# Kernel tuning notes

Measured on AMD Instinct MI355X. Metric: run time of the kernel, lower is better.

Reference implementation:

```python
import jax, jax.numpy as jnp
import numpy as np

N_NODES = 50000
HID = 256


def _gcn_norm(edge_index, n_nodes):
    # PyG GCNConv default: add self-loops, symmetric normalization
    src, dst = edge_index[0], edge_index[1]
    loop = jnp.arange(n_nodes, dtype=src.dtype)
    src = jnp.concatenate([src, loop])
    dst = jnp.concatenate([dst, loop])
    deg = jax.ops.segment_sum(jnp.ones_like(src, dtype=jnp.float32), dst, num_segments=n_nodes)
    dinv = jnp.where(deg > 0, jax.lax.rsqrt(jnp.maximum(deg, 1.0)), 0.0)
    norm = dinv[src] * dinv[dst]  # [E + N]
    return src, dst, norm


def _gcn_conv(x, W, b, src, dst, norm, n_nodes):
    h = x @ W                                   # [N, H] dense transform first (PyG order)
    msg = h[src] * norm[:, None]                # gather + scale
    out = jax.ops.segment_sum(msg, dst, num_segments=n_nodes)
    return out + b


def setup_inputs() -> dict:
    key = jax.random.key(0)
    ks = jax.random.split(key, 8)
    x = jax.random.normal(ks[0], (N_NODES, HID), dtype=jnp.float32)
    edge_index = jax.random.randint(ks[1], (2, 1600000), 0, N_NODES, dtype=jnp.int64)
    s = 1.0 / np.sqrt(HID)
    W1 = jax.random.normal(ks[2], (HID, HID), dtype=jnp.float32) * s
    b1 = jnp.zeros((HID,), dtype=jnp.float32)
    Wmu = jax.random.normal(ks[3], (HID, HID), dtype=jnp.float32) * s
    bmu = jnp.zeros((HID,), dtype=jnp.float32)
    Wls = jax.random.normal(ks[4], (HID, HID), dtype=jnp.float32) * s * 0.1
    bls = jnp.zeros((HID,), dtype=jnp.float32)
    return {"x": x, "edge_index": edge_index, "W1": W1, "b1": b1,
            "Wmu": Wmu, "bmu": bmu, "Wls": Wls, "bls": bls}


def reference(x, edge_index, W1, b1, Wmu, bmu, Wls, bls):
    n = x.shape[0]
    src, dst, norm = _gcn_norm(edge_index, n)
    h = jax.nn.relu(_gcn_conv(x, W1, b1, src, dst, norm, n))
    mu = _gcn_conv(h, Wmu, bmu, src, dst, norm, n)
    logstd = _gcn_conv(h, Wls, bls, src, dst, norm, n)
    std = jnp.exp(logstd)
    eps = jax.random.normal(jax.random.key(1), std.shape, dtype=std.dtype)
    z = mu + std * eps
    return (z, mu, logstd)
```

## Files before the change

kernel.cpp:

```cpp
#include <hip/hip_runtime.h>
#include <stdint.h>

#define HID 256

typedef __bf16 bf16x8 __attribute__((ext_vector_type(8)));
typedef float  f32x4  __attribute__((ext_vector_type(4)));
typedef unsigned int uint4v __attribute__((ext_vector_type(4)));

__device__ __forceinline__ unsigned short f2bf(float f){
  unsigned int x = __float_as_uint(f);
  x += 0x7FFFu + ((x >> 16) & 1u);
  return (unsigned short)(x >> 16);
}
__device__ __forceinline__ float bf2f(unsigned int u){
  return __uint_as_float(u << 16);
}
__device__ __forceinline__ bf16x8 ntload8(const unsigned short* p){
  uint4v t = __builtin_nontemporal_load((const uint4v*)p);
  return __builtin_bit_cast(bf16x8, t);
}

__global__ void count_kernel(const int* __restrict__ ei, int E, int* __restrict__ deg){
  int e = blockIdx.x*256 + threadIdx.x;
  if (e < E) atomicAdd(&deg[ei[E + e]], 1);
}

__global__ void dinv_kernel(const int* __restrict__ deg, float* __restrict__ dinv, int N){
  int i = blockIdx.x*256 + threadIdx.x;
  if (i < N) dinv[i] = 1.0f / sqrtf((float)(deg[i] + 1));
}

__global__ void scan1_kernel(const int* __restrict__ deg, int* __restrict__ rowptr,
                             int* __restrict__ partials, int N){
  __shared__ int sm[256];
  int t = threadIdx.x;
  int i = blockIdx.x*256 + t;
  int v = (i < N) ? deg[i] : 0;
  int acc = v;
  sm[t] = acc;
  __syncthreads();
  for (int off = 1; off < 256; off <<= 1){
    int add = (t >= off) ? sm[t - off] : 0;
    __syncthreads();
    acc += add;
    sm[t] = acc;
    __syncthreads();
  }
  if (i < N) rowptr[i] = acc - v;
  if (t == 255) partials[blockIdx.x] = acc;
}

__global__ void scan2_kernel(int* __restrict__ partials, int nb){
  __shared__ int sm[256];
  int t = threadIdx.x;
  int v = (t < nb) ? partials[t] : 0;
  int acc = v;
  sm[t] = acc;
  __syncthreads();
  for (int off = 1; off < 256; off <<= 1){
    int add = (t >= off) ? sm[t - off] : 0;
    __syncthreads();
    acc += add;
    sm[t] = acc;
    __syncthreads();
  }
  if (t < nb) partials[t] = acc - v;
}

__global__ void scan3_kernel(int* __restrict__ rowptr, const int* __restrict__ partials,
                             int N, int E){
  int i = blockIdx.x*256 + threadIdx.x;
  if (i < N) rowptr[i] += partials[blockIdx.x];
  if (i == 0) rowptr[N] = E;
}

__global__ void scatter_kernel(const int* __restrict__ ei, int E, const int* __restrict__ rowptr,
                               int* __restrict__ fill, const float* __restrict__ dinv,
                               int* __restrict__ col, float* __restrict__ wgt){
  int e = blockIdx.x*256 + threadIdx.x;
  if (e >= E) return;
  int s = ei[e];
  int d = ei[E + e];
  int p = rowptr[d] + atomicAdd(&fill[d], 1);
  col[p] = s;
  wgt[p] = dinv[s] * dinv[d];
}

__global__ void convX_kernel(const float* __restrict__ x, unsigned short* __restrict__ xb, int total8){
  int t = blockIdx.x*256 + threadIdx.x;
  if (t >= total8) return;
  const float* p = x + (size_t)t*8;
  f32x4 a = *(const f32x4*)p;
  f32x4 b = *(const f32x4*)(p + 4);
  ushort4 o0, o1;
  o0.x = f2bf(a[0]); o0.y = f2bf(a[1]); o0.z = f2bf(a[2]); o0.w = f2bf(a[3]);
  o1.x = f2bf(b[0]); o1.y = f2bf(b[1]); o1.z = f2bf(b[2]); o1.w = f2bf(b[3]);
  ushort4* q = (ushort4*)(xb + (size_t)t*8);
  q[0] = o0; q[1] = o1;
}

__global__ void convW_kernel(const float* __restrict__ W1, const float* __restrict__ Wmu,
                             const float* __restrict__ Wls, unsigned short* __restrict__ Wt){
  int t = blockIdx.x*256 + threadIdx.x;
  if (t >= 3*65536) return;
  int m = t >> 16;
  int r = t & 0xFFFF;
  int n = r >> 8, k = r & 255;
  int ksrc = (m == 0) ? k : ((k & ~63) | ((k & 3) << 4) | ((k >> 2) & 15));
  const float* W = (m == 0) ? W1 : (m == 1 ? Wmu : Wls);
  Wt[t] = f2bf(W[ksrc*HID + n]);
}

__global__ void agg_bf16(const unsigned short* __restrict__ X, unsigned short* __restrict__ Y,
                         const int* __restrict__ rowptr, const int* __restrict__ col,
                         const float* __restrict__ wgt, const float* __restrict__ dinv,
                         int N, int sin, int sout){
  int w = (blockIdx.x * blockDim.x + threadIdx.x) >> 6;
  int lane = threadIdx.x & 63;
  if (w >= N) return;
  float sd = dinv[w];
  f32x4 acc;
  {
    uint2 u = *((const uint2*)(X + (size_t)w*sin) + lane);
    float s2 = sd*sd;
    acc[0] = bf2f(u.x & 0xFFFFu) * s2;
    acc[1] = bf2f(u.x >> 16)     * s2;
    acc[2] = bf2f(u.y & 0xFFFFu) * s2;
    acc[3] = bf2f(u.y >> 16)     * s2;
  }
  int p0 = rowptr[w], p1 = rowptr[w+1];
  for (int base = p0; base < p1; base += 64){
    int idx = base + lane;
    int   sc = 0;  float wc = 0.f;
    if (idx < p1){ sc = col[idx]; wc = wgt[idx]; }
    int cnt = min(p1 - base, 64);
    for (int j = 0; j < cnt; ++j){
      int   s = __shfl(sc, j);
      float f = __shfl(wc, j);
      uint2 u = *((const uint2*)(X + (size_t)s*sin) + lane);
      acc[0] = fmaf(bf2f(u.x & 0xFFFFu), f, acc[0]);
      acc[1] = fmaf(bf2f(u.x >> 16),     f, acc[1]);
      acc[2] = fmaf(bf2f(u.y & 0xFFFFu), f, acc[2]);
      acc[3] = fmaf(bf2f(u.y >> 16),     f, acc[3]);
    }
  }
  ushort4 o;
  o.x = f2bf(acc[0]); o.y = f2bf(acc[1]); o.z = f2bf(acc[2]); o.w = f2bf(acc[3]);
  *((ushort4*)(Y + (size_t)w*sout) + lane) = o;
}

__global__ __launch_bounds__(256, 4) void gemm1_kernel(const unsigned short* __restrict__ A,
    const unsigned short* __restrict__ Bt, const float* __restrict__ bias,
    unsigned short* __restrict__ H, int N){
  int r0 = blockIdx.x * 32;
  int lane = threadIdx.x & 63;
  int nw = threadIdx.x >> 6;
  int lr = lane & 15, kg = lane >> 4;
  f32x4 acc[2][4] = {};
  for (int ks = 0; ks < 8; ++ks){
    int kb = ks*32 + kg*8;
    bf16x8 af[2];
    #pragma unroll
    for (int rf = 0; rf < 2; ++rf){
      int row = r0 + rf*16 + lr; if (row > N-1) row = N-1;
      af[rf] = *(const bf16x8*)(A + (size_t)row*HID + kb);
    }
    #pragma unroll
    for (int cf = 0; cf < 4; ++cf){
      int c = nw*64 + cf*16 + lr;
      bf16x8 bfr = *(const bf16x8*)(Bt + (size_t)c*HID + kb);
      acc[0][cf] = __builtin_amdgcn_mfma_f32_16x16x32_bf16(af[0], bfr, acc[0][cf], 0, 0, 0);
      acc[1][cf] = __builtin_amdgcn_mfma_f32_16x16x32_bf16(af[1], bfr, acc[1][cf], 0, 0, 0);
    }
  }
  float bv[4];
  #pragma unroll
  for (int cf = 0; cf < 4; ++cf) bv[cf] = bias[nw*64 + cf*16 + lr];
  #pragma unroll
  for (int rf = 0; rf < 2; ++rf){
    #pragma unroll
    for (int i = 0; i < 4; ++i){
      int row = r0 + rf*16 + kg*4 + i;
      if (row < N){
        ushort4 o;
        o.x = f2bf(fmaxf(acc[rf][0][i] + bv[0], 0.0f));
        o.y = f2bf(fmaxf(acc[rf][1][i] + bv[1], 0.0f));
        o.z = f2bf(fmaxf(acc[rf][2][i] + bv[2], 0.0f));
        o.w = f2bf(fmaxf(acc[rf][3][i] + bv[3], 0.0f));
        *(ushort4*)(H + (size_t)row*HID + nw*64 + lr*4) = o;
      }
    }
  }
}

__device__ __forceinline__ unsigned int rotl32(unsigned int v, int r){
  return (v << r) | (v >> (32 - r));
}

__device__ __forceinline__ float gauss_eps(unsigned int idxv){
  unsigned int x0 = 0u, x1 = idxv;
  const unsigned int ks0 = 0u, ks1 = 1u, ks2 = 0x1BD11BDAu ^ 0u ^ 1u;
  x0 += ks0; x1 += ks1;
#define TFR(r) { x0 += x1; x1 = rotl32(x1, r); x1 ^= x0; }
  TFR(13) TFR(15) TFR(26) TFR(6)   x0 += ks1; x1 += ks2 + 1u;
  TFR(17) TFR(29) TFR(16) TFR(24)  x0 += ks2; x1 += ks0 + 2u;
  TFR(13) TFR(15) TFR(26) TFR(6)   x0 += ks0; x1 += ks1 + 3u;
  TFR(17) TFR(29) TFR(16) TFR(24)  x0 += ks1; x1 += ks2 + 4u;
  TFR(13) TFR(15) TFR(26) TFR(6)   x0 += ks2; x1 += ks0 + 5u;
#undef TFR
  unsigned int bits = x0 ^ x1;
  float f = __uint_as_float((bits >> 9) | 0x3F800000u) - 1.0f;
  const float lo = -0.99999994f;
  float u = fmaxf(lo, fmaf(f, 2.0f, lo));
  float t = fmaf(-u, u, 1.0f);
  float wv = -0.69314718056f * __builtin_amdgcn_logf(t);
  float p;
  if (wv < 5.0f){
    wv -= 2.5f;
    p = 2.81022636e-08f;
    p = fmaf(p, wv, 3.43273939e-07f);
    p = fmaf(p, wv, -3.5233877e-06f);
    p = fmaf(p, wv, -4.39150654e-06f);
    p = fmaf(p, wv, 0.00021858087f);
    p = fmaf(p, wv, -0.00125372503f);
    p = fmaf(p, wv, -0.00417768164f);
    p = fmaf(p, wv, 0.246640727f);
    p = fmaf(p, wv, 1.50140941f);
  } else {
    wv = sqrtf(wv) - 3.0f;
    p = -0.000200214257f;
    p = fmaf(p, wv, 0.000100950558f);
    p = fmaf(p, wv, 0.00134934322f);
    p = fmaf(p, wv, -0.00367342844f);
    p = fmaf(p, wv, 0.00573950773f);
    p = fmaf(p, wv, -0.0076224613f);
    p = fmaf(p, wv, 0.00943887047f);
    p = fmaf(p, wv, 1.00167406f);
    p = fmaf(p, wv, 2.83297682f);
  }
  return 1.4142135381698608f * (p * u);
}

__global__ __launch_bounds__(256, 4) void gemm23_kernel(const unsigned short* __restrict__ A2b,
    const unsigned short* __restrict__ Btm, const unsigned short* __restrict__ Btl,
    const float* __restrict__ bmu, const float* __restrict__ bls,
    float* __restrict__ Z, float* __restrict__ MU, float* __restrict__ LS, int N){
  __shared__ float sml[2][16][260];
  int r0 = blockIdx.x * 32;
  int lane = threadIdx.x & 63;
  int nw = threadIdx.x >> 6;
  int lr = lane & 15, kg = lane >> 4;
  f32x4 am[2][4] = {};
  f32x4 al[2][4] = {};
  for (int ks = 0; ks < 8; ++ks){
    int kb = ks*32 + kg*8;
    bf16x8 af[2];
    #pragma unroll
    for (int rf = 0; rf < 2; ++rf){
      int row = r0 + rf*16 + lr; if (row > N-1) row = N-1;
      af[rf] = ntload8(A2b + (size_t)row*512 + kb);
    }
    #pragma unroll
    for (int cf = 0; cf < 4; ++cf){
      int c = nw*64 + cf*16 + lr;
      bf16x8 bm_ = *(const bf16x8*)(Btm + (size_t)c*HID + kb);
      bf16x8 bl_ = *(const bf16x8*)(Btl + (size_t)c*HID + kb);
      am[0][cf] = __builtin_amdgcn_mfma_f32_16x16x32_bf16(af[0], bm_, am[0][cf], 0, 0, 0);
      am[1][cf] = __builtin_amdgcn_mfma_f32_16x16x32_bf16(af[1], bm_, am[1][cf], 0, 0, 0);
      al[0][cf] = __builtin_amdgcn_mfma_f32_16x16x32_bf16(af[0], bl_, al[0][cf], 0, 0, 0);
      al[1][cf] = __builtin_amdgcn_mfma_f32_16x16x32_bf16(af[1], bl_, al[1][cf], 0, 0, 0);
    }
  }
  f32x4 bm4 = *(const f32x4*)(bmu + lane*4);
  f32x4 bl4 = *(const f32x4*)(bls + lane*4);
  for (int rf = 0; rf < 2; ++rf){
    #pragma unroll
    for (int cf = 0; cf < 4; ++cf){
      int c = nw*64 + cf*16 + lr;
      #pragma unroll
      for (int i = 0; i < 4; ++i){
        int rl = kg*4 + i;
        sml[0][rl][c] = am[rf][cf][i];
        sml[1][rl][c] = al[rf][cf][i];
      }
    }
    __syncthreads();
    #pragma unroll
    for (int rr = 0; rr < 4; ++rr){
      int rl = nw*4 + rr;
      int row = r0 + rf*16 + rl;
      if (row < N){
        f32x4 m4 = *(const f32x4*)&sml[0][rl][lane*4];
        f32x4 l4 = *(const f32x4*)&sml[1][rl][lane*4];
        m4 += bm4;
        l4 += bl4;
        size_t base = (size_t)row*HID + lane*4;
        f32x4 z4;
        #pragma unroll
        for (int j = 0; j < 4; ++j){
          float e = gauss_eps((unsigned int)(base + j));
          float s = __builtin_amdgcn_exp2f(l4[j] * 1.44269504f);
          z4[j] = fmaf(s, e, m4[j]);
        }
        __builtin_nontemporal_store(z4, (f32x4*)(Z  + base));
        __builtin_nontemporal_store(m4, (f32x4*)(MU + base));
        __builtin_nontemporal_store(l4, (f32x4*)(LS + base));
      }
    }
    __syncthreads();
  }
}

extern "C" void kernel_launch(void* const* d_in, const int* in_sizes, int n_in,
                              void* d_out, int out_size, void* d_ws, size_t ws_size,
                              hipStream_t stream){
  const float* x   = (const float*)d_in[0];
  const int*   ei  = (const int*)d_in[1];
  const float* W1  = (const float*)d_in[2];
  const float* b1  = (const float*)d_in[3];
  const float* Wmu = (const float*)d_in[4];
  const float* bmu = (const float*)d_in[5];
  const float* Wls = (const float*)d_in[6];
  const float* bls = (const float*)d_in[7];
  const int N = in_sizes[0] / HID;
  const int E = in_sizes[1] / 2;
  const size_t NA = ((size_t)N + 64) & ~(size_t)63;

  int* deg      = (int*)d_ws;
  int* fill     = deg + NA;
  int* rowptr   = fill + NA;
  int* partials = rowptr + NA;
  float* dinv   = (float*)(partials + 1024);
  int*  col     = (int*)(dinv + NA);
  float* wgt    = (float*)(col + (size_t)E);
  unsigned short* Wt = (unsigned short*)(wgt + (size_t)E);

  float* Z  = (float*)d_out;
  float* MU = Z + (size_t)N*HID;
  float* LS = MU + (size_t)N*HID;
  unsigned short* hb  = (unsigned short*)Z;
  unsigned short* xb  = (unsigned short*)Z + (size_t)N*HID;
  unsigned short* a1b = (unsigned short*)MU;
  unsigned short* a2b = (unsigned short*)LS;

  hipMemsetAsync(deg, 0, NA*2*sizeof(int), stream);

  int ebl = (E + 255)/256, nbl = (N + 255)/256;
  count_kernel  <<<ebl, 256, 0, stream>>>(ei, E, deg);
  dinv_kernel   <<<nbl, 256, 0, stream>>>(deg, dinv, N);
  scan1_kernel  <<<nbl, 256, 0, stream>>>(deg, rowptr, partials, N);
  scan2_kernel  <<<1,   256, 0, stream>>>(partials, nbl);
  scan3_kernel  <<<nbl, 256, 0, stream>>>(rowptr, partials, N, E);
  scatter_kernel<<<ebl, 256, 0, stream>>>(ei, E, rowptr, fill, dinv, col, wgt);
  convW_kernel  <<<768, 256, 0, stream>>>(W1, Wmu, Wls, Wt);
  convX_kernel  <<<(N*HID/8 + 255)/256, 256, 0, stream>>>(x, xb, N*HID/8);

  agg_bf16    <<<(N + 3)/4,  256, 0, stream>>>(xb, a1b, rowptr, col, wgt, dinv, N, 256, 256);
  gemm1_kernel<<<(N + 31)/32, 256, 0, stream>>>(a1b, Wt, b1, hb, N);
  agg_bf16    <<<(N + 3)/4,  256, 0, stream>>>(hb, a2b, rowptr, col, wgt, dinv, N, 256, 512);
  gemm23_kernel<<<(N + 31)/32, 256, 0, stream>>>(a2b, Wt + 65536, Wt + 2*65536,
                                                 bmu, bls, Z, MU, LS, N);
}
```

Before: 793.8 us.

## Widen aggregation gathers to 16B with half-wave edge split; cut gemm LDS

In the aggregation kernel, each half-wave now handles alternate edges and each lane loads 16 bytes (8 bf16) instead of 8 bytes. The two halves are combined with a cross-half shuffle before the store, which halves the number of gather iterations per wave. The gemm23 epilogue now reuses a single LDS tile twice, staging mu then logstd, and the launch bounds rise to allow higher occupancy. The second aggregation writes into spare workspace at stride 256 when ws_size is large enough, otherwise it keeps the strided output buffer. The price is extra syncthreads, a lane-reduction shuffle and added register pressure under the tighter occupancy bounds.

Result: slower. 920.9 us (+16.0%).

```diff
diff --git a/kernel.cpp b/kernel.cpp
--- a/kernel.cpp
+++ b/kernel.cpp
@@ -15,6 +15,8 @@
 __device__ __forceinline__ float bf2f(unsigned int u){
   return __uint_as_float(u << 16);
 }
+__device__ __forceinline__ float bflo(unsigned int x){ return __uint_as_float(x << 16); }
+__device__ __forceinline__ float bfhi(unsigned int x){ return __uint_as_float(x & 0xFFFF0000u); }
 __device__ __forceinline__ bf16x8 ntload8(const unsigned short* p){
   uint4v t = __builtin_nontemporal_load((const uint4v*)p);
   return __builtin_bit_cast(bf16x8, t);
@@ -118,38 +120,48 @@
   int w = (blockIdx.x * blockDim.x + threadIdx.x) >> 6;
   int lane = threadIdx.x & 63;
   if (w >= N) return;
-  float sd = dinv[w];
-  f32x4 acc;
-  {
-    uint2 u = *((const uint2*)(X + (size_t)w*sin) + lane);
-    float s2 = sd*sd;
-    acc[0] = bf2f(u.x & 0xFFFFu) * s2;
-    acc[1] = bf2f(u.x >> 16)     * s2;
-    acc[2] = bf2f(u.y & 0xFFFFu) * s2;
-    acc[3] = bf2f(u.y >> 16)     * s2;
+  int half = lane >> 5, cl = lane & 31;
+  float acc[8];
+  if (half == 0){
+    float s2 = dinv[w]; s2 *= s2;
+    uint4v u = *(const uint4v*)(X + (size_t)w*sin + cl*8);
+    acc[0]=bflo(u.x)*s2; acc[1]=bfhi(u.x)*s2; acc[2]=bflo(u.y)*s2; acc[3]=bfhi(u.y)*s2;
+    acc[4]=bflo(u.z)*s2; acc[5]=bfhi(u.z)*s2; acc[6]=bflo(u.w)*s2; acc[7]=bfhi(u.w)*s2;
+  } else {
+    #pragma unroll
+    for (int k = 0; k < 8; ++k) acc[k] = 0.f;
   }
   int p0 = rowptr[w], p1 = rowptr[w+1];
   for (int base = p0; base < p1; base += 64){
     int idx = base + lane;
-    int   sc = 0;  float wc = 0.f;
+    int sc = 0; float wc = 0.f;
     if (idx < p1){ sc = col[idx]; wc = wgt[idx]; }
     int cnt = min(p1 - base, 64);
-    for (int j = 0; j < cnt; ++j){
-      int   s = __shfl(sc, j);
-      float f = __shfl(wc, j);
-      uint2 u = *((const uint2*)(X + (size_t)s*sin) + lane);
-      acc[0] = fmaf(bf2f(u.x & 0xFFFFu), f, acc[0]);
-      acc[1] = fmaf(bf2f(u.x >> 16),     f, acc[1]);
-      acc[2] = fmaf(bf2f(u.y & 0xFFFFu), f, acc[2]);
-      acc[3] = fmaf(bf2f(u.y >> 16),     f, acc[3]);
-    }
-  }
-  ushort4 o;
-  o.x = f2bf(acc[0]); o.y = f2bf(acc[1]); o.z = f2bf(acc[2]); o.w = f2bf(acc[3]);
-  *((ushort4*)(Y + (size_t)w*sout) + lane) = o;
-}
-
-__global__ __launch_bounds__(256, 4) void gemm1_kernel(const unsigned short* __restrict__ A,
+    for (int j = 0; j < cnt; j += 2){
+      int   s0 = __shfl(sc, j),   s1 = __shfl(sc, j+1);
+      float f0 = __shfl(wc, j),   f1 = __shfl(wc, j+1);
+      int   s = half ? s1 : s0;
+      float f = half ? f1 : f0;
+      uint4v u = *(const uint4v*)(X + (size_t)s*sin + cl*8);
+      acc[0]=fmaf(bflo(u.x),f,acc[0]); acc[1]=fmaf(bfhi(u.x),f,acc[1]);
+      acc[2]=fmaf(bflo(u.y),f,acc[2]); acc[3]=fmaf(bfhi(u.y),f,acc[3]);
+      acc[4]=fmaf(bflo(u.z),f,acc[4]); acc[5]=fmaf(bfhi(u.z),f,acc[5]);
+      acc[6]=fmaf(bflo(u.w),f,acc[6]); acc[7]=fmaf(bfhi(u.w),f,acc[7]);
+    }
+  }
+  #pragma unroll
+  for (int k = 0; k < 8; ++k) acc[k] += __shfl_xor(acc[k], 32);
+  if (half == 0){
+    uint4v o;
+    o.x = (unsigned int)f2bf(acc[0]) | ((unsigned int)f2bf(acc[1]) << 16);
+    o.y = (unsigned int)f2bf(acc[2]) | ((unsigned int)f2bf(acc[3]) << 16);
+    o.z = (unsigned int)f2bf(acc[4]) | ((unsigned int)f2bf(acc[5]) << 16);
+    o.w = (unsigned int)f2bf(acc[6]) | ((unsigned int)f2bf(acc[7]) << 16);
+    *(uint4v*)(Y + (size_t)w*sout + cl*8) = o;
+  }
+}
+
+__global__ __launch_bounds__(256, 8) void gemm1_kernel(const unsigned short* __restrict__ A,
     const unsigned short* __restrict__ Bt, const float* __restrict__ bias,
     unsigned short* __restrict__ H, int N){
   int r0 = blockIdx.x * 32;
@@ -241,11 +253,11 @@
   return 1.4142135381698608f * (p * u);
 }
 
-__global__ __launch_bounds__(256, 4) void gemm23_kernel(const unsigned short* __restrict__ A2b,
+__global__ __launch_bounds__(256, 6) void gemm23_kernel(const unsigned short* __restrict__ A2b,
     const unsigned short* __restrict__ Btm, const unsigned short* __restrict__ Btl,
     const float* __restrict__ bmu, const float* __restrict__ bls,
-    float* __restrict__ Z, float* __restrict__ MU, float* __restrict__ LS, int N){
-  __shared__ float sml[2][16][260];
+    float* __restrict__ Z, float* __restrict__ MU, float* __restrict__ LS, int N, int sa){
+  __shared__ float sml[16][260];
   int r0 = blockIdx.x * 32;
   int lane = threadIdx.x & 63;
   int nw = threadIdx.x >> 6;
@@ -258,7 +270,7 @@
     #pragma unroll
     for (int rf = 0; rf < 2; ++rf){
       int row = r0 + rf*16 + lr; if (row > N-1) row = N-1;
-      af[rf] = ntload8(A2b + (size_t)row*512 + kb);
+      af[rf] = ntload8(A2b + (size_t)row*sa + kb);
     }
     #pragma unroll
     for (int cf = 0; cf < 4; ++cf){
@@ -278,11 +290,18 @@
     for (int cf = 0; cf < 4; ++cf){
       int c = nw*64 + cf*16 + lr;
       #pragma unroll
-      for (int i = 0; i < 4; ++i){
-        int rl = kg*4 + i;
-        sml[0][rl][c] = am[rf][cf][i];
-        sml[1][rl][c] = al[rf][cf][i];
-      }
+      for (int i = 0; i < 4; ++i) sml[kg*4 + i][c] = am[rf][cf][i];
+    }
+    __syncthreads();
+    f32x4 m4[4];
+    #pragma unroll
+    for (int rr = 0; rr < 4; ++rr) m4[rr] = *(const f32x4*)&sml[nw*4 + rr][lane*4];
+    __syncthreads();
+    #pragma unroll
+    for (int cf = 0; cf < 4; ++cf){
+      int c = nw*64 + cf*16 + lr;
+      #pragma unroll
+      for (int i = 0; i < 4; ++i) sml[kg*4 + i][c] = al[rf][cf][i];
     }
     __syncthreads();
     #pragma unroll
@@ -290,21 +309,20 @@
       int rl = nw*4 + rr;
       int row = r0 + rf*16 + rl;
       if (row < N){
-        f32x4 m4 = *(const f32x4*)&sml[0][rl][lane*4];
-        f32x4 l4 = *(const f32x4*)&sml[1][rl][lane*4];
-        m4 += bm4;
-        l4 += bl4;
+        f32x4 l4 = *(const f32x4*)&sml[rl][lane*4];
+        f32x4 m = m4[rr] + bm4;
+        f32x4 l = l4 + bl4;
         size_t base = (size_t)row*HID + lane*4;
         f32x4 z4;
         #pragma unroll
         for (int j = 0; j < 4; ++j){
           float e = gauss_eps((unsigned int)(base + j));
-          float s = __builtin_amdgcn_exp2f(l4[j] * 1.44269504f);
-          z4[j] = fmaf(s, e, m4[j]);
+          float s = __builtin_amdgcn_exp2f(l[j] * 1.44269504f);
+          z4[j] = fmaf(s, e, m[j]);
         }
         __builtin_nontemporal_store(z4, (f32x4*)(Z  + base));
-        __builtin_nontemporal_store(m4, (f32x4*)(MU + base));
-        __builtin_nontemporal_store(l4, (f32x4*)(LS + base));
+        __builtin_nontemporal_store(m,  (f32x4*)(MU + base));
+        __builtin_nontemporal_store(l,  (f32x4*)(LS + base));
       }
     }
     __syncthreads();
@@ -334,6 +352,7 @@
   int*  col     = (int*)(dinv + NA);
   float* wgt    = (float*)(col + (size_t)E);
   unsigned short* Wt = (unsigned short*)(wgt + (size_t)E);
+  unsigned short* a2ws = Wt + 3*65536;
 
   float* Z  = (float*)d_out;
   float* MU = Z + (size_t)N*HID;
@@ -341,7 +360,11 @@
   unsigned short* hb  = (unsigned short*)Z;
   unsigned short* xb  = (unsigned short*)Z + (size_t)N*HID;
   unsigned short* a1b = (unsigned short*)MU;
-  unsigned short* a2b = (unsigned short*)LS;
+
+  size_t ws_used = (size_t)((char*)a2ws - (char*)d_ws);
+  bool packed = (ws_size >= ws_used + (size_t)N * 256 * sizeof(unsigned short));
+  unsigned short* a2b = packed ? a2ws : (unsigned short*)LS;
+  int sa = packed ? 256 : 512;
 
   hipMemsetAsync(deg, 0, NA*2*sizeof(int), stream);
 
@@ -355,9 +378,9 @@
   convW_kernel  <<<768, 256, 0, stream>>>(W1, Wmu, Wls, Wt);
   convX_kernel  <<<(N*HID/8 + 255)/256, 256, 0, stream>>>(x, xb, N*HID/8);
 
-  agg_bf16    <<<(N + 3)/4,  256, 0, stream>>>(xb, a1b, rowptr, col, wgt, dinv, N, 256, 256);
-  gemm1_kernel<<<(N + 31)/32, 256, 0, stream>>>(a1b, Wt, b1, hb, N);
-  agg_bf16    <<<(N + 3)/4,  256, 0, stream>>>(hb, a2b, rowptr, col, wgt, dinv, N, 256, 512);
+  agg_bf16     <<<(N + 3)/4,  256, 0, stream>>>(xb, a1b, rowptr, col, wgt, dinv, N, 256, 256);
+  gemm1_kernel <<<(N + 31)/32, 256, 0, stream>>>(a1b, Wt, b1, hb, N);
+  agg_bf16     <<<(N + 3)/4,  256, 0, stream>>>(hb, a2b, rowptr, col, wgt, dinv, N, 256, sa);
   gemm23_kernel<<<(N + 31)/32, 256, 0, stream>>>(a2b, Wt + 65536, Wt + 2*65536,
-                                                 bmu, bls, Z, MU, LS, N);
-}
+                                                 bmu, bls, Z, MU, LS, N, sa);
+}
```
